# Optimization experiments

Hardware: AMD Instinct MI355X
Metric: run time of the kernel (lower is better)

## Reference

```python
import jax, jax.numpy as jnp
import numpy as np

D_MODEL = 1024
NUM_HEADS = 16
DEPTH = D_MODEL // NUM_HEADS


def setup_inputs() -> dict:
    key = jax.random.key(0)
    ks = jax.random.split(key, 9)
    B, S = 2, 2048
    scale = 1.0 / np.sqrt(D_MODEL)
    x = jax.random.normal(ks[0], (B, S, D_MODEL), dtype=jnp.float32)
    wq = jax.random.normal(ks[1], (D_MODEL, D_MODEL), dtype=jnp.float32) * scale
    bq = jax.random.normal(ks[2], (D_MODEL,), dtype=jnp.float32) * 0.01
    wk = jax.random.normal(ks[3], (D_MODEL, D_MODEL), dtype=jnp.float32) * scale
    bk = jax.random.normal(ks[4], (D_MODEL,), dtype=jnp.float32) * 0.01
    wv = jax.random.normal(ks[5], (D_MODEL, D_MODEL), dtype=jnp.float32) * scale
    bv = jax.random.normal(ks[6], (D_MODEL,), dtype=jnp.float32) * 0.01
    wo = jax.random.normal(ks[7], (D_MODEL, D_MODEL), dtype=jnp.float32) * scale
    bo = jax.random.normal(ks[8], (D_MODEL,), dtype=jnp.float32) * 0.01
    return {"x": x, "wq": wq, "bq": bq, "wk": wk, "bk": bk,
            "wv": wv, "bv": bv, "wo": wo, "bo": bo}


def reference(x, wq, bq, wk, bk, wv, bv, wo, bo):
    B, S, _ = x.shape
    def split_heads(t):  # [B,S,D] -> [B,H,S,depth]
        return t.reshape(B, S, NUM_HEADS, DEPTH).transpose(0, 2, 1, 3)
    q = split_heads(x @ wq + bq)
    k = split_heads(x @ wk + bk)
    v = split_heads(x @ wv + bv)
    # scaled dot-product attention, full [B,H,S,S] scores as in the original
    logits = jnp.einsum('bhqd,bhkd->bhqk', q, k) / jnp.sqrt(
        jnp.asarray(DEPTH, dtype=jnp.float32))
    attn = jax.nn.softmax(logits, axis=-1)
    out = jnp.einsum('bhqk,bhkd->bhqd', attn, v)
    out = out.transpose(0, 2, 1, 3).reshape(B, S, D_MODEL)
    return out @ wo + bo
```

## Files before the change

### kernel.cpp

```cpp
#include <hip/hip_runtime.h>


#define S_LEN 2048
#define DM 1024
#define MROWS 4096
#define QSCALE 0.1803368801111244f

typedef unsigned short u16;
typedef unsigned int u32;
typedef __attribute__((ext_vector_type(8))) short short8;
typedef __attribute__((ext_vector_type(4))) float f32x4;
typedef __attribute__((ext_vector_type(4))) unsigned short u16x4;

__device__ inline u16 f2bf(float f) {
    u32 u = __float_as_uint(f);
    u = u + 0x7fffu + ((u >> 16) & 1u);
    return (u16)(u >> 16);
}
__device__ inline void gld_lds16(const u16* g, u16* l) {
    __builtin_amdgcn_global_load_lds(
        (const __attribute__((address_space(1))) void*)g,
        (__attribute__((address_space(3))) void*)l, 16, 0, 0);
}
__device__ inline f32x4 mfma16(short8 a, short8 b, f32x4 c) {
    return __builtin_amdgcn_mfma_f32_16x16x32_bf16(a, b, c, 0, 0, 0);
}

__global__ void prep_all(const float* __restrict__ x, u16* __restrict__ xb,
                         const float* __restrict__ wq, const float* __restrict__ wk,
                         const float* __restrict__ wv, const float* __restrict__ wo,
                         const float* __restrict__ bq, const float* __restrict__ bk,
                         const float* __restrict__ bv, const float* __restrict__ bo,
                         u16* __restrict__ wallT, u16* __restrict__ woT,
                         float* __restrict__ biasAll, float* __restrict__ biasO) {
    const int t = threadIdx.x;
    if (blockIdx.x < 2048) {
        const size_t i8 = ((size_t)blockIdx.x * 256 + t) * 8;
        const f32x4 a = ((const f32x4*)x)[i8 / 4];
        const f32x4 b = ((const f32x4*)x)[i8 / 4 + 1];
        u16 o[8];
#pragma unroll
        for (int i = 0; i < 4; i++) { o[i] = f2bf(a[i]); o[4 + i] = f2bf(b[i]); }
        *(short8*)(xb + i8) = *(const short8*)o;
        return;
    }
    const int bid = blockIdx.x - 2048;
    if (bid == 1024) {
#pragma unroll
        for (int i = 0; i < 4; i++) {
            const int idx = i * 256 + t;
            biasAll[idx]        = bq[idx] * QSCALE;
            biasAll[1024 + idx] = bk[idx];
            biasAll[2048 + idx] = bv[idx];
            biasO[idx]          = bo[idx];
        }
        return;
    }
    __shared__ float lds[64][65];
    const int m  = bid >> 8;
    const int tk = (bid >> 4) & 15;
    const int tn = bid & 15;
    const float* src = (m == 0) ? wq : (m == 1) ? wk : (m == 2) ? wv : wo;
    const float scale = (m == 0) ? QSCALE : 1.0f;
    const int r4 = t >> 6, c = t & 63;
#pragma unroll
    for (int i = 0; i < 16; i++) {
        const int k = tk * 64 + i * 4 + r4;
        lds[i * 4 + r4][c] = src[(size_t)k * 1024 + tn * 64 + c];
    }
    __syncthreads();
#pragma unroll
    for (int i = 0; i < 16; i++) {
        const int n = tn * 64 + i * 4 + r4;
        const int k = tk * 64 + c;
        const u16 v = f2bf(lds[c][i * 4 + r4] * scale);
        if (m < 3) wallT[((size_t)m * 1024 + n) * 1024 + k] = v;
        else       woT[(size_t)n * 1024 + k] = v;
    }
}

__global__ __launch_bounds__(256, 2)
void gemm_qkv(const u16* __restrict__ A, const u16* __restrict__ Bt,
              const float* __restrict__ bias, u16* __restrict__ Cq,
              u16* __restrict__ Ck, u16* __restrict__ Cv,
              const int K, const int N) {
    __shared__ __align__(16) u16 As[128 * 32];
    __shared__ __align__(16) u16 Bs[128 * 32];
    const int tid = threadIdx.x;
    const int w = tid >> 6, lane = tid & 63;
    const int wm = w >> 1, wn = w & 1;
    const int l16 = lane & 15, quad = lane >> 4;
    const int tm = blockIdx.x * 128;
    const int tn = blockIdx.y * 128;
    const int region = tn >> 10;

    const int sr = w * 16 + (lane >> 2);
    const int sc = (lane & 3) * 8;
    const u16* ag0 = A + (size_t)(tm + sr) * K + sc;
    const u16* ag1 = A + (size_t)(tm + sr + 64) * K + sc;
    const u16* bg0 = Bt + (size_t)(tn + sr) * K + sc;
    const u16* bg1 = Bt + (size_t)(tn + sr + 64) * K + sc;
    u16* al = As + w * 512;
    u16* bl = Bs + w * 512;

    f32x4 acc[4][4];
#pragma unroll
    for (int i = 0; i < 4; i++)
#pragma unroll
        for (int j = 0; j < 4; j++) acc[i][j] = (f32x4){0.f, 0.f, 0.f, 0.f};

    for (int kb = 0; kb < K; kb += 32) {
        __syncthreads();
        gld_lds16(ag0 + kb, al);
        gld_lds16(ag1 + kb, al + 2048);
        gld_lds16(bg0 + kb, bl);
        gld_lds16(bg1 + kb, bl + 2048);
        __syncthreads();
        short8 af[4], bfr[4];
#pragma unroll
        for (int i = 0; i < 4; i++) {
            af[i]  = *(const short8*)(As + (wm * 64 + i * 16 + l16) * 32 + quad * 8);
            bfr[i] = *(const short8*)(Bs + (wn * 64 + i * 16 + l16) * 32 + quad * 8);
        }
#pragma unroll
        for (int i = 0; i < 4; i++)
#pragma unroll
            for (int j = 0; j < 4; j++)
                acc[i][j] = mfma16(af[i], bfr[j], acc[i][j]);
    }
#pragma unroll
    for (int j = 0; j < 4; j++) {
        const int col = tn + wn * 64 + j * 16 + l16;
        const float bv = bias[col];
#pragma unroll
        for (int i = 0; i < 4; i++) {
            const int row0 = tm + wm * 64 + i * 16 + quad * 4;
#pragma unroll
            for (int r = 0; r < 4; r++) {
                const u16 vb = f2bf(acc[i][j][r] + bv);
                const int row = row0 + r;
                if (region == 0) {
                    Cq[(size_t)row * 1024 + col] = vb;
                } else if (region == 1) {
                    const int s = row & 2047, b = row >> 11;
                    const int hd = col - 1024, h = hd >> 6, d = hd & 63;
                    Ck[(((size_t)(b * 16 + h) * 2048 + s) << 6) +
                       (((d >> 3) + s) & 7) * 8 + (d & 7)] = vb;
                } else {
                    const int s = row & 2047, b = row >> 11;
                    const int hd = col - 2048, h = hd >> 6, d = hd & 63;
                    const int sl = s & 63;
                    const int p = (sl & 32) | ((sl & 15) << 1) | ((sl >> 4) & 1);
                    const int phys = ((((p >> 3) + d) & 7) << 3) | (p & 7);
                    Cv[(((size_t)((b * 16 + h) * 32 + (s >> 6))) << 12) +
                       d * 64 + phys] = vb;
                }
            }
        }
    }
}

__global__ __launch_bounds__(256, 2)
void gemm_out64(const u16* __restrict__ A, const u16* __restrict__ Bt,
                const float* __restrict__ bias, float* __restrict__ C,
                const int K, const int N) {
    __shared__ __align__(16) u16 As[64 * 32];
    __shared__ __align__(16) u16 Bs[128 * 32];
    const int tid = threadIdx.x;
    const int w = tid >> 6, lane = tid & 63;
    const int wm = w >> 1, wn = w & 1;
    const int l16 = lane & 15, quad = lane >> 4;
    const int tm = blockIdx.x * 64;
    const int tn = blockIdx.y * 128;

    const int sr = w * 16 + (lane >> 2);
    const int sc = (lane & 3) * 8;
    const u16* ag  = A + (size_t)(tm + sr) * K + sc;
    const u16* bg0 = Bt + (size_t)(tn + sr) * K + sc;
    const u16* bg1 = Bt + (size_t)(tn + sr + 64) * K + sc;
    u16* al = As + w * 512;
    u16* bl = Bs + w * 512;

    f32x4 acc[2][4];
#pragma unroll
    for (int i = 0; i < 2; i++)
#pragma unroll
        for (int j = 0; j < 4; j++) acc[i][j] = (f32x4){0.f, 0.f, 0.f, 0.f};

    for (int kb = 0; kb < K; kb += 32) {
        __syncthreads();
        gld_lds16(ag + kb, al);
        gld_lds16(bg0 + kb, bl);
        gld_lds16(bg1 + kb, bl + 2048);
        __syncthreads();
        short8 af[2], bfr[4];
#pragma unroll
        for (int i = 0; i < 2; i++)
            af[i] = *(const short8*)(As + (wm * 32 + i * 16 + l16) * 32 + quad * 8);
#pragma unroll
        for (int j = 0; j < 4; j++)
            bfr[j] = *(const short8*)(Bs + (wn * 64 + j * 16 + l16) * 32 + quad * 8);
#pragma unroll
        for (int i = 0; i < 2; i++)
#pragma unroll
            for (int j = 0; j < 4; j++)
                acc[i][j] = mfma16(af[i], bfr[j], acc[i][j]);
    }
#pragma unroll
    for (int j = 0; j < 4; j++) {
        const int col = tn + wn * 64 + j * 16 + l16;
        const float bv = bias[col];
#pragma unroll
        for (int i = 0; i < 2; i++) {
            const int row0 = tm + wm * 32 + i * 16 + quad * 4;
#pragma unroll
            for (int r = 0; r < 4; r++)
                C[(size_t)(row0 + r) * N + col] = acc[i][j][r] + bv;
        }
    }
}

__global__ __launch_bounds__(128, 2)
void flash_attn(const u16* __restrict__ Qb, const u16* __restrict__ Ktg,
                const u16* __restrict__ Vtb, u16* __restrict__ O) {
    __shared__ __align__(16) u16 Ks[4096];
    __shared__ __align__(16) u16 Vs[4096];
    const int tid = threadIdx.x;
    const int w = tid >> 6, lane = tid & 63;
    const int l16 = lane & 15, quad = lane >> 4;
    const int bh = blockIdx.y, b = bh >> 4, h = bh & 15;
    const int q0 = blockIdx.x * 64 + w * 32;

    short8 qf[2][2];
#pragma unroll
    for (int u = 0; u < 2; u++) {
        const size_t qrow = (size_t)(b * S_LEN + q0 + u * 16 + l16) * 1024 + h * 64;
        qf[u][0] = *(const short8*)(Qb + qrow + quad * 8);
        qf[u][1] = *(const short8*)(Qb + qrow + 32 + quad * 8);
    }
    u16 ones_s[8];
#pragma unroll
    for (int i = 0; i < 8; i++) ones_s[i] = 0x3F80u;
    const short8 ones = *(const short8*)ones_s;

    const u16* kg = Ktg + ((size_t)bh << 17) + w * 2048 + lane * 8;
    const u16* vg = Vtb + ((size_t)bh << 17) + w * 2048 + lane * 8;
    u16* kl = Ks + w * 2048;
    u16* vl = Vs + w * 2048;

    const int ka0 = l16 * 64 + ((quad + l16) & 7) * 8;
    const int ka1 = l16 * 64 + ((4 + quad + l16) & 7) * 8;

    f32x4 o[2][4], osum[2];
#pragma unroll
    for (int u = 0; u < 2; u++) {
        osum[u] = (f32x4){0.f, 0.f, 0.f, 0.f};
#pragma unroll
        for (int d = 0; d < 4; d++) o[u][d] = (f32x4){0.f, 0.f, 0.f, 0.f};
    }
    const f32x4 zz = (f32x4){0.f, 0.f, 0.f, 0.f};

    for (int t = 0; t < S_LEN / 64; t++) {
        __syncthreads();
        const int off = t * 4096;
        gld_lds16(kg + off,        kl);
        gld_lds16(kg + off + 512,  kl + 512);
        gld_lds16(kg + off + 1024, kl + 1024);
        gld_lds16(kg + off + 1536, kl + 1536);
        gld_lds16(vg + off,        vl);
        gld_lds16(vg + off + 512,  vl + 512);
        gld_lds16(vg + off + 1024, vl + 1024);
        gld_lds16(vg + off + 1536, vl + 1536);
        __syncthreads();

        f32x4 s[2][4];
#pragma unroll
        for (int a = 0; a < 4; a++) {
            const short8 kf0 = *(const short8*)(Ks + a * 1024 + ka0);
            const short8 kf1 = *(const short8*)(Ks + a * 1024 + ka1);
#pragma unroll
            for (int u = 0; u < 2; u++) {
                s[u][a] = mfma16(kf0, qf[u][0], zz);
                s[u][a] = mfma16(kf1, qf[u][1], s[u][a]);
            }
        }
        union { u32 u[4]; short8 s8; } pu[2][2];
#pragma unroll
        for (int u = 0; u < 2; u++) {
#pragma unroll
            for (int r = 0; r < 4; r++) {
                const float e0 = __builtin_amdgcn_exp2f(s[u][0][r]);
                const float e1 = __builtin_amdgcn_exp2f(s[u][1][r]);
                const float e2 = __builtin_amdgcn_exp2f(s[u][2][r]);
                const float e3 = __builtin_amdgcn_exp2f(s[u][3][r]);
                pu[u][0].u[r] = __builtin_amdgcn_perm(
                    __float_as_uint(e1), __float_as_uint(e0), 0x07060302u);
                pu[u][1].u[r] = __builtin_amdgcn_perm(
                    __float_as_uint(e3), __float_as_uint(e2), 0x07060302u);
            }
            osum[u] = mfma16(ones, pu[u][0].s8, osum[u]);
            osum[u] = mfma16(ones, pu[u][1].s8, osum[u]);
        }
#pragma unroll
        for (int dv = 0; dv < 4; dv++) {
            const short8 vf0 = *(const short8*)(Vs + dv * 1024 + ka0);
            const short8 vf1 = *(const short8*)(Vs + dv * 1024 + ka1);
#pragma unroll
            for (int u = 0; u < 2; u++) {
                o[u][dv] = mfma16(vf0, pu[u][0].s8, o[u][dv]);
                o[u][dv] = mfma16(vf1, pu[u][1].s8, o[u][dv]);
            }
        }
    }

#pragma unroll
    for (int u = 0; u < 2; u++) {
        const float inv = 1.0f / osum[u][0];
        const size_t obase =
            (size_t)(b * S_LEN + q0 + u * 16 + l16) * DM + h * 64 + quad * 4;
#pragma unroll
        for (int d = 0; d < 4; d++) {
            u16x4 pk;
#pragma unroll
            for (int r = 0; r < 4; r++) pk[r] = f2bf(o[u][d][r] * inv);
            *(u16x4*)(O + obase + d * 16) = pk;
        }
    }
}

extern "C" void kernel_launch(void* const* d_in, const int* in_sizes, int n_in,
                              void* d_out, int out_size, void* d_ws, size_t ws_size,
                              hipStream_t stream) {
    const float* x  = (const float*)d_in[0];
    const float* wq = (const float*)d_in[1];
    const float* bq = (const float*)d_in[2];
    const float* wk = (const float*)d_in[3];
    const float* bk = (const float*)d_in[4];
    const float* wv = (const float*)d_in[5];
    const float* bv = (const float*)d_in[6];
    const float* wo = (const float*)d_in[7];
    const float* bo = (const float*)d_in[8];

    char* ws = (char*)d_ws;
    u16*   wallT   = (u16*)(ws + 64);
    u16*   woT     = (u16*)(ws + 6291520);
    float* biasAll = (float*)(ws + 8388672);
    float* biasO   = (float*)(ws + 8400960);
    u16*   xb      = (u16*)(ws + 8405056);
    u16*   Qb      = (u16*)(ws + 16793664);
    u16*   Ktg     = (u16*)(ws + 25182272);
    u16*   Vtb     = (u16*)(ws + 33570880);
    u16*   Obuf    = (u16*)(ws + 41959488);

    prep_all<<<3073, 256, 0, stream>>>(x, xb, wq, wk, wv, wo, bq, bk, bv, bo,
                                       wallT, woT, biasAll, biasO);
    gemm_qkv<<<dim3(32, 24), 256, 0, stream>>>(xb, wallT, biasAll,
                                               Qb, Ktg, Vtb, 1024, 3072);
    flash_attn<<<dim3(32, 32), 128, 0, stream>>>(Qb, Ktg, Vtb, Obuf);
    gemm_out64<<<dim3(64, 8), 256, 0, stream>>>(Obuf, woT, biasO,
                                                (float*)d_out, 1024, 1024);
}
```

Baseline: 195.9 us.

## Stage QKV epilogue through LDS for vectorized stores; widen attention blocks to 4 waves

The QKV GEMM epilogue now writes bias-added bf16 results into a padded LDS tile and then emits 16-byte vector stores into the Q, swizzled K and permuted V layouts. Previously these were scattered 2-byte stores. Flash attention now runs 256 threads per block covering 128 queries, so each K/V tile loaded into LDS is shared by four waves instead of two, halving global K/V traffic per query. In exchange, the GEMM uses about 34 KB more LDS per block, which may lower occupancy, and the attention grid has half as many blocks.

```diff
diff --git a/kernel.cpp b/kernel.cpp
--- a/kernel.cpp
+++ b/kernel.cpp
@@ -11,6 +11,7 @@
 typedef __attribute__((ext_vector_type(8))) short short8;
 typedef __attribute__((ext_vector_type(4))) float f32x4;
 typedef __attribute__((ext_vector_type(4))) unsigned short u16x4;
+typedef __attribute__((ext_vector_type(2))) unsigned int u32x2;
 
 __device__ inline u16 f2bf(float f) {
     u32 u = __float_as_uint(f);
@@ -86,6 +87,7 @@
               const int K, const int N) {
     __shared__ __align__(16) u16 As[128 * 32];
     __shared__ __align__(16) u16 Bs[128 * 32];
+    __shared__ __align__(16) u16 Ct[128 * 136];
     const int tid = threadIdx.x;
     const int w = tid >> 6, lane = tid & 63;
     const int wm = w >> 1, wn = w & 1;
@@ -128,34 +130,80 @@
             for (int j = 0; j < 4; j++)
                 acc[i][j] = mfma16(af[i], bfr[j], acc[i][j]);
     }
-#pragma unroll
-    for (int j = 0; j < 4; j++) {
-        const int col = tn + wn * 64 + j * 16 + l16;
-        const float bv = bias[col];
-#pragma unroll
-        for (int i = 0; i < 4; i++) {
-            const int row0 = tm + wm * 64 + i * 16 + quad * 4;
-#pragma unroll
-            for (int r = 0; r < 4; r++) {
-                const u16 vb = f2bf(acc[i][j][r] + bv);
-                const int row = row0 + r;
-                if (region == 0) {
-                    Cq[(size_t)row * 1024 + col] = vb;
-                } else if (region == 1) {
-                    const int s = row & 2047, b = row >> 11;
-                    const int hd = col - 1024, h = hd >> 6, d = hd & 63;
-                    Ck[(((size_t)(b * 16 + h) * 2048 + s) << 6) +
-                       (((d >> 3) + s) & 7) * 8 + (d & 7)] = vb;
-                } else {
-                    const int s = row & 2047, b = row >> 11;
-                    const int hd = col - 2048, h = hd >> 6, d = hd & 63;
-                    const int sl = s & 63;
-                    const int p = (sl & 32) | ((sl & 15) << 1) | ((sl >> 4) & 1);
-                    const int phys = ((((p >> 3) + d) & 7) << 3) | (p & 7);
-                    Cv[(((size_t)((b * 16 + h) * 32 + (s >> 6))) << 12) +
-                       d * 64 + phys] = vb;
-                }
+
+    if (region < 2) {
+#pragma unroll
+        for (int j = 0; j < 4; j++) {
+            const int colL = wn * 64 + j * 16 + l16;
+            const float bv = bias[tn + colL];
+#pragma unroll
+            for (int i = 0; i < 4; i++) {
+                const int row0 = wm * 64 + i * 16 + quad * 4;
+#pragma unroll
+                for (int r = 0; r < 4; r++)
+                    Ct[(row0 + r) * 136 + colL] = f2bf(acc[i][j][r] + bv);
             }
+        }
+    } else {
+#pragma unroll
+        for (int j = 0; j < 4; j++) {
+            const int colL = wn * 64 + j * 16 + l16;
+            const float bv = bias[tn + colL];
+#pragma unroll
+            for (int i = 0; i < 4; i++) {
+                const int row0 = wm * 64 + i * 16 + quad * 4;
+                u16x4 pk;
+#pragma unroll
+                for (int r = 0; r < 4; r++) pk[r] = f2bf(acc[i][j][r] + bv);
+                *(u16x4*)(Ct + colL * 132 + row0) = pk;
+            }
+        }
+    }
+    __syncthreads();
+
+    if (region == 0) {
+#pragma unroll
+        for (int p = 0; p < 8; p++) {
+            const int rowL = p * 16 + (tid >> 4);
+            const int c8 = (tid & 15) * 8;
+            const short8 v = *(const short8*)(Ct + rowL * 136 + c8);
+            *(short8*)(Cq + (size_t)(tm + rowL) * 1024 + tn + c8) = v;
+        }
+    } else if (region == 1) {
+        const int b = tm >> 11, sBase = tm & 2047;
+#pragma unroll
+        for (int p = 0; p < 8; p++) {
+            const int rowL = p * 16 + (tid >> 4);
+            const int c8 = (tid & 15) * 8;
+            const short8 v = *(const short8*)(Ct + rowL * 136 + c8);
+            const int s = sBase + rowL;
+            const int hd = (tn - 1024) + c8;
+            const int h = hd >> 6, dd = hd & 63;
+            const int chunk = ((dd >> 3) + s) & 7;
+            *(short8*)(Ck + (((size_t)(b * 16 + h) * 2048 + s) << 6) + chunk * 8) = v;
+        }
+    } else {
+        const int b = tm >> 11, tBase = (tm & 2047) >> 6;
+        const int hBase = (tn >> 6) - 32;
+#pragma unroll
+        for (int p = 0; p < 8; p++) {
+            const int cid = p * 256 + tid;
+            const int q3 = cid & 7;
+            const int colL = (cid >> 3) & 127;
+            const int half = cid >> 10;
+            const int d = colL & 63;
+            const int h = hBase + (colL >> 6);
+            const int c = (q3 - d) & 7;
+            const int base = (c & 3) * 4 + ((c & 4) << 3);
+            const u32x2 Ar = *(const u32x2*)(Ct + colL * 132 + half * 64 + base);
+            const u32x2 Br = *(const u32x2*)(Ct + colL * 132 + half * 64 + base + 16);
+            union { u32 u[4]; short8 s8; } o;
+            o.u[0] = __builtin_amdgcn_perm(Br[0], Ar[0], 0x05040100u);
+            o.u[1] = __builtin_amdgcn_perm(Br[0], Ar[0], 0x07060302u);
+            o.u[2] = __builtin_amdgcn_perm(Br[1], Ar[1], 0x05040100u);
+            o.u[3] = __builtin_amdgcn_perm(Br[1], Ar[1], 0x07060302u);
+            *(short8*)(Cv + (((size_t)((b * 16 + h) * 32 + tBase + half)) << 12) +
+                       d * 64 + q3 * 8) = o.s8;
         }
     }
 }
@@ -220,7 +268,7 @@
     }
 }
 
-__global__ __launch_bounds__(128, 2)
+__global__ __launch_bounds__(256, 2)
 void flash_attn(const u16* __restrict__ Qb, const u16* __restrict__ Ktg,
                 const u16* __restrict__ Vtb, u16* __restrict__ O) {
     __shared__ __align__(16) u16 Ks[4096];
@@ -229,7 +277,7 @@
     const int w = tid >> 6, lane = tid & 63;
     const int l16 = lane & 15, quad = lane >> 4;
     const int bh = blockIdx.y, b = bh >> 4, h = bh & 15;
-    const int q0 = blockIdx.x * 64 + w * 32;
+    const int q0 = blockIdx.x * 128 + w * 32;
 
     short8 qf[2][2];
 #pragma unroll
@@ -243,10 +291,10 @@
     for (int i = 0; i < 8; i++) ones_s[i] = 0x3F80u;
     const short8 ones = *(const short8*)ones_s;
 
-    const u16* kg = Ktg + ((size_t)bh << 17) + w * 2048 + lane * 8;
-    const u16* vg = Vtb + ((size_t)bh << 17) + w * 2048 + lane * 8;
-    u16* kl = Ks + w * 2048;
-    u16* vl = Vs + w * 2048;
+    const u16* kg = Ktg + ((size_t)bh << 17) + w * 1024 + lane * 8;
+    const u16* vg = Vtb + ((size_t)bh << 17) + w * 1024 + lane * 8;
+    u16* kl = Ks + w * 1024;
+    u16* vl = Vs + w * 1024;
 
     const int ka0 = l16 * 64 + ((quad + l16) & 7) * 8;
     const int ka1 = l16 * 64 + ((4 + quad + l16) & 7) * 8;
@@ -263,14 +311,10 @@
     for (int t = 0; t < S_LEN / 64; t++) {
         __syncthreads();
         const int off = t * 4096;
-        gld_lds16(kg + off,        kl);
-        gld_lds16(kg + off + 512,  kl + 512);
-        gld_lds16(kg + off + 1024, kl + 1024);
-        gld_lds16(kg + off + 1536, kl + 1536);
-        gld_lds16(vg + off,        vl);
-        gld_lds16(vg + off + 512,  vl + 512);
-        gld_lds16(vg + off + 1024, vl + 1024);
-        gld_lds16(vg + off + 1536, vl + 1536);
+        gld_lds16(kg + off,       kl);
+        gld_lds16(kg + off + 512, kl + 512);
+        gld_lds16(vg + off,       vl);
+        gld_lds16(vg + off + 512, vl + 512);
         __syncthreads();
 
         f32x4 s[2][4];
@@ -356,7 +400,7 @@
                                        wallT, woT, biasAll, biasO);
     gemm_qkv<<<dim3(32, 24), 256, 0, stream>>>(xb, wallT, biasAll,
                                                Qb, Ktg, Vtb, 1024, 3072);
-    flash_attn<<<dim3(32, 32), 128, 0, stream>>>(Qb, Ktg, Vtb, Obuf);
+    flash_attn<<<dim3(16, 32), 256, 0, stream>>>(Qb, Ktg, Vtb, Obuf);
     gemm_out64<<<dim3(64, 8), 256, 0, stream>>>(Obuf, woT, biasO,
                                                 (float*)d_out, 1024, 1024);
 }
```

New measurement: 181.4 us. -7.4%, faster.
